# Kernel optimization log

Measured on AMD Instinct MI355X. Metric: run time of the kernel, lower is better.

The kernel has to match this reference:

```python
import jax, jax.numpy as jnp
import numpy as np

N_NODES, D = 10000, 128
N_EDGES = 640000
BN_EPS = 1e-3  # keras BatchNormalization default


def _bn(x, gamma, beta, mean, var):
    return (x - mean) * jax.lax.rsqrt(var + BN_EPS) * gamma + beta


def _ffn_block(x, gamma, beta, mean, var, W, b):
    # BatchNorm (inference) -> Dropout (identity at inference) -> Dense + gelu (exact, keras default)
    return jax.nn.gelu(_bn(x, gamma, beta, mean, var) @ W + b, approximate=False)


def setup_inputs() -> dict:
    key = jax.random.key(0)
    ks = jax.random.split(key, 32)
    inp = {
        "node_features": jax.random.normal(ks[0], (N_NODES, D), jnp.float32),
        "edges": jax.random.randint(ks[1], (2, N_EDGES), 0, N_NODES, jnp.int64),
        "edge_weights": jax.random.uniform(ks[2], (N_EDGES,), jnp.float32),
    }
    def bn_params(i, dim, prefix):
        return {
            prefix + "_g": jnp.ones((dim,), jnp.float32) + 0.1 * jax.random.normal(ks[i], (dim,)),
            prefix + "_b": 0.1 * jax.random.normal(ks[i + 1], (dim,)),
            prefix + "_m": 0.1 * jax.random.normal(ks[i + 2], (dim,)),
            prefix + "_v": jax.random.uniform(ks[i + 3], (dim,), minval=0.5, maxval=1.5),
        }
    def dense_params(i, din, dout, prefix):
        s = (2.0 / (din + dout)) ** 0.5
        return {
            prefix + "_W": s * jax.random.normal(ks[i], (din, dout), jnp.float32),
            prefix + "_bias": jnp.zeros((dout,), jnp.float32),
        }
    # prepare FFN: BN(D)->Dense(D->128), BN(128)->Dense(128->128)
    inp.update(bn_params(3, D, "p1")); inp.update(dense_params(7, D, 128, "p1"))
    inp.update(bn_params(8, 128, "p2")); inp.update(dense_params(12, 128, 128, "p2"))
    # update FFN (concat -> 2*D input): BN(2D)->Dense(2D->128), BN(128)->Dense(128->128)
    inp.update(bn_params(13, 2 * D, "u1")); inp.update(dense_params(17, 2 * D, 128, "u1"))
    inp.update(bn_params(18, 128, "u2")); inp.update(dense_params(22, 128, 128, "u2"))
    return inp


def reference(node_features, edges, edge_weights,
              p1_g, p1_b, p1_m, p1_v, p1_W, p1_bias,
              p2_g, p2_b, p2_m, p2_v, p2_W, p2_bias,
              u1_g, u1_b, u1_m, u1_v, u1_W, u1_bias,
              u2_g, u2_b, u2_m, u2_v, u2_W, u2_bias):
    num_nodes = node_features.shape[0]
    node_idx, nbr_idx = edges[0], edges[1]
    # gather neighbor representations [E, D]
    neigh = node_features[nbr_idx]
    # prepare: ffn on neighbors, then scale by edge weights
    msg = _ffn_block(neigh, p1_g, p1_b, p1_m, p1_v, p1_W, p1_bias)
    msg = _ffn_block(msg, p2_g, p2_b, p2_m, p2_v, p2_W, p2_bias)
    msg = msg * edge_weights[:, None]
    # aggregate: unsorted_segment_mean
    agg = jax.ops.segment_sum(msg, node_idx, num_segments=num_nodes)
    cnt = jax.ops.segment_sum(jnp.ones_like(edge_weights), node_idx, num_segments=num_nodes)
    agg = agg / jnp.maximum(cnt, 1.0)[:, None]
    # update: concat + ffn
    h = jnp.concatenate([node_features, agg], axis=1)
    h = _ffn_block(h, u1_g, u1_b, u1_m, u1_v, u1_W, u1_bias)
    h = _ffn_block(h, u2_g, u2_b, u2_m, u2_v, u2_W, u2_bias)
    return h
```

## Files before the change

kernel.cpp:

```cpp
#include <hip/hip_runtime.h>
#include <hip/hip_bf16.h>
#include <hip/hip_fp16.h>
#include <math.h>

#define N_NODES 10000
#define DIM 128
#define N_EDGES 640000
#define BN_EPS 1e-3f

#define QUARTER 2500
#define PART_BLOCKS 250
#define EDGES_PER_PART 2560
#define HIST_GRID 1000
#define MSG64_BLOCKS 157
#define SU_BLOCKS 1250
#define HIST_PAD 10240

typedef _Float16 half8 __attribute__((ext_vector_type(8)));
typedef float f32x4 __attribute__((ext_vector_type(4)));

__device__ __forceinline__ float gelu_exact(float x) {
  return 0.5f * x * (1.0f + erff(x * 0.70710678f));
}

__device__ __forceinline__ int lds_swz(int row, int colbyte) {
  return ((row * 256 + colbyte) ^ ((row & 7) << 4));
}

struct FoldAll {
  const float* g[4];
  const float* bb[4];
  const float* m[4];
  const float* v[4];
  const float* W[4];
  const float* bias[4];
  _Float16* pk[4];
  float* bf[4];
  int din[4];
  int S[4];
};

__global__ __launch_bounds__(256) void fold_hist_kernel(FoldAll fa,
                                                        const int* __restrict__ node_idx,
                                                        unsigned char* __restrict__ part) {
  __shared__ int lh[QUARTER];
  __shared__ float t_sh[256];
  __shared__ float bpart[128];
  int b = blockIdx.x, t = threadIdx.x;
  if (b >= 44) {
    int pb = b - 44;
    int eb = pb >> 2;
    int q = pb & 3;
    int qbase = q * QUARTER;
    for (int i = t; i < QUARTER; i += 256) lh[i] = 0;
    __syncthreads();
    int base0 = eb * EDGES_PER_PART;
#pragma unroll
    for (int s = 0; s < 3; ++s) {
      int off = s * 1024 + t * 4;
      if (off < EDGES_PER_PART) {
        int4 vv = *reinterpret_cast<const int4*>(&node_idx[base0 + off]);
        unsigned d0 = (unsigned)(vv.x - qbase);
        unsigned d1 = (unsigned)(vv.y - qbase);
        unsigned d2 = (unsigned)(vv.z - qbase);
        unsigned d3 = (unsigned)(vv.w - qbase);
        if (d0 < QUARTER) atomicAdd(&lh[d0], 1);
        if (d1 < QUARTER) atomicAdd(&lh[d1], 1);
        if (d2 < QUARTER) atomicAdd(&lh[d2], 1);
        if (d3 < QUARTER) atomicAdd(&lh[d3], 1);
      }
    }
    __syncthreads();
    unsigned char* prow = part + (size_t)(q * PART_BLOCKS + eb) * QUARTER;
    for (int i = t; i < QUARTER; i += 256) prow[i] = (unsigned char)lh[i];
    return;
  }
  if (b >= 40) {
    int p = b - 40;
    int din = fa.din[p];
    const float* W = fa.W[p];
    for (int k = t; k < din; k += 256) {
      float sc = fa.g[p][k] * rsqrtf(fa.v[p][k] + BN_EPS);
      t_sh[k] = fa.bb[p][k] - fa.m[p][k] * sc;
    }
    __syncthreads();
    int j = t & 127, kh = t >> 7;
    int half = din >> 1;
    float acc = 0.f;
    for (int k = kh * half; k < (kh + 1) * half; ++k)
      acc = fmaf(t_sh[k], W[k * 128 + j], acc);
    if (kh == 1) bpart[j] = acc;
    __syncthreads();
    if (kh == 0) fa.bf[p][j] = acc + bpart[j] + fa.bias[p][j];
    return;
  }
  int p, lf;
  if (b < 8)       { p = 0; lf = b * 256 + t; }
  else if (b < 16) { p = 1; lf = (b - 8) * 256 + t; }
  else if (b < 32) { p = 2; lf = (b - 16) * 256 + t; }
  else             { p = 3; lf = (b - 32) * 256 + t; }
  int S = fa.S[p];
  int l = lf & 63;
  int fs = lf >> 6;
  int f = fs & 7, s = fs >> 3;
  if (s >= S) return;
  const float* W = fa.W[p];
  const float* g = fa.g[p];
  const float* v = fa.v[p];
  int k0 = s * 32 + (l >> 4) * 8;
  int col = f * 16 + (l & 15);
  half8 h;
#pragma unroll
  for (int i = 0; i < 8; ++i) {
    int k = k0 + i;
    float sc = g[k] * rsqrtf(v[k] + BN_EPS);
    h[i] = (_Float16)(sc * W[k * 128 + col]);
  }
  *reinterpret_cast<half8*>(fa.pk[p] + (size_t)lf * 8) = h;
}

__global__ __launch_bounds__(256) void merge_msg_kernel(
    unsigned char* __restrict__ part, int* __restrict__ hist,
    const float* __restrict__ x,
    const _Float16* __restrict__ W1pk, const float* __restrict__ b1f,
    const _Float16* __restrict__ W2pk, const float* __restrict__ b2f,
    _Float16* __restrict__ M) {
  __shared__ char lds_raw[4 * 4096];
  int b = blockIdx.x, t = threadIdx.x;
  if (b < 40) {
    int bin = b * 256 + t;
    if (bin < N_NODES) {
      int q = bin / QUARTER;
      int bp = bin - q * QUARTER;
      unsigned char* col = part + (size_t)q * PART_BLOCKS * QUARTER + bp;
      int sum = 0;
#pragma unroll
      for (int c = 0; c < PART_BLOCKS; c += 25) {
        int vals[25];
#pragma unroll
        for (int i = 0; i < 25; ++i) vals[i] = col[(size_t)(c + i) * QUARTER];
#pragma unroll
        for (int i = 0; i < 25; ++i) {
          col[(size_t)(c + i) * QUARTER] = (unsigned char)sum;
          sum += vals[i];
        }
      }
      hist[bin] = sum;
    } else if (bin < HIST_PAD) {
      hist[bin] = 0;
    }
    return;
  }
  int wid = t >> 6, lane = t & 63;
  int r = lane & 15, g = lane >> 4;
  int row0 = (b - 40) * 64 + wid * 16;
  char* lbase = lds_raw + wid * 4096;

  int arow = row0 + r;
  if (arow > N_NODES - 1) arow = N_NODES - 1;
  const float* xp = x + (size_t)arow * DIM;

  half8 a[4];
#pragma unroll
  for (int s = 0; s < 4; ++s) {
    float4 lo = *reinterpret_cast<const float4*>(xp + s * 32 + g * 8);
    float4 hi = *reinterpret_cast<const float4*>(xp + s * 32 + g * 8 + 4);
    half8 h;
    h[0] = (_Float16)lo.x; h[1] = (_Float16)lo.y; h[2] = (_Float16)lo.z; h[3] = (_Float16)lo.w;
    h[4] = (_Float16)hi.x; h[5] = (_Float16)hi.y; h[6] = (_Float16)hi.z; h[7] = (_Float16)hi.w;
    a[s] = h;
  }

  f32x4 zero = {0.f, 0.f, 0.f, 0.f};
  f32x4 acc[8];
#pragma unroll
  for (int f = 0; f < 8; ++f) acc[f] = zero;
#pragma unroll
  for (int f = 0; f < 8; ++f)
#pragma unroll
    for (int s = 0; s < 4; ++s) {
      half8 bfrag = *reinterpret_cast<const half8*>(W1pk + (size_t)((s * 8 + f) * 64 + lane) * 8);
      acc[f] = __builtin_amdgcn_mfma_f32_16x16x32_f16(a[s], bfrag, acc[f], 0, 0, 0);
    }

#pragma unroll
  for (int f = 0; f < 8; ++f) {
    int col = f * 16 + r;
    float bv = b1f[col];
#pragma unroll
    for (int j = 0; j < 4; ++j) {
      int rl = g * 4 + j;
      float gv = gelu_exact(acc[f][j] + bv);
      *reinterpret_cast<_Float16*>(lbase + lds_swz(rl, col * 2)) = (_Float16)gv;
    }
  }

  half8 a2[4];
#pragma unroll
  for (int s = 0; s < 4; ++s)
    a2[s] = *reinterpret_cast<const half8*>(lbase + lds_swz(r, (s * 32 + g * 8) * 2));

  f32x4 acc2[8];
#pragma unroll
  for (int f = 0; f < 8; ++f) acc2[f] = zero;
#pragma unroll
  for (int f = 0; f < 8; ++f)
#pragma unroll
    for (int s = 0; s < 4; ++s) {
      half8 bfrag = *reinterpret_cast<const half8*>(W2pk + (size_t)((s * 8 + f) * 64 + lane) * 8);
      acc2[f] = __builtin_amdgcn_mfma_f32_16x16x32_f16(a2[s], bfrag, acc2[f], 0, 0, 0);
    }

#pragma unroll
  for (int f = 0; f < 8; ++f) {
    int col = f * 16 + r;
    float bv = b2f[col];
#pragma unroll
    for (int j = 0; j < 4; ++j) {
      int grow = row0 + g * 4 + j;
      if (grow < N_NODES)
        M[(size_t)grow * DIM + col] = (_Float16)gelu_exact(acc2[f][j] + bv);
    }
  }
}

__global__ __launch_bounds__(256) void scatter_kernel(
    const int* __restrict__ node_idx, const int* __restrict__ nbr_idx,
    const float* __restrict__ ew, const int* __restrict__ hist,
    const unsigned char* __restrict__ part, uint2* __restrict__ edge_s,
    int* __restrict__ row_start) {
  __shared__ int cur[QUARTER];
  __shared__ int sums[256];
  int bk = blockIdx.x, t = threadIdx.x;
  int eb = bk >> 2;
  int q = bk & 3;
  int qbase = q * QUARTER;
  const int PER = 40;
  int i0 = t * PER;
  int lh[PER];
  int total = 0;
#pragma unroll
  for (int i = 0; i < PER; i += 4) {
    int4 h4 = *reinterpret_cast<const int4*>(&hist[i0 + i]);
    lh[i] = h4.x; lh[i + 1] = h4.y; lh[i + 2] = h4.z; lh[i + 3] = h4.w;
    total += h4.x + h4.y + h4.z + h4.w;
  }
  sums[t] = total;
  __syncthreads();
  for (int off = 1; off < 256; off <<= 1) {
    int v = (t >= off) ? sums[t - off] : 0;
    __syncthreads();
    sums[t] += v;
    __syncthreads();
  }
  int running = sums[t] - total;
  const unsigned char* prow = part + (size_t)(q * PART_BLOCKS + eb) * QUARTER;
  bool wrs = (bk == 0);
#pragma unroll
  for (int i = 0; i < PER; ++i) {
    int idx = i0 + i;
    if (idx < N_NODES) {
      unsigned d = (unsigned)(idx - qbase);
      if (d < QUARTER) cur[d] = running + (int)prow[d];
      if (wrs) row_start[idx] = running;
      running += lh[i];
    }
  }
  if (wrs && t == 255) row_start[N_NODES] = running;
  __syncthreads();

  int base0 = eb * EDGES_PER_PART;
#pragma unroll
  for (int s = 0; s < 3; ++s) {
    int off = s * 1024 + t * 4;
    if (off >= EDGES_PER_PART) break;
    int base = base0 + off;
    int4 ni = *reinterpret_cast<const int4*>(&node_idx[base]);
    int4 nb = *reinterpret_cast<const int4*>(&nbr_idx[base]);
    float4 wv = *reinterpret_cast<const float4*>(&ew[base]);
    unsigned d0 = (unsigned)(ni.x - qbase);
    unsigned d1 = (unsigned)(ni.y - qbase);
    unsigned d2 = (unsigned)(ni.z - qbase);
    unsigned d3 = (unsigned)(ni.w - qbase);
    if (d0 < QUARTER) {
      int p0 = atomicAdd(&cur[d0], 1);
      edge_s[p0] = make_uint2((unsigned)nb.x, __float_as_uint(wv.x));
    }
    if (d1 < QUARTER) {
      int p1 = atomicAdd(&cur[d1], 1);
      edge_s[p1] = make_uint2((unsigned)nb.y, __float_as_uint(wv.y));
    }
    if (d2 < QUARTER) {
      int p2 = atomicAdd(&cur[d2], 1);
      edge_s[p2] = make_uint2((unsigned)nb.z, __float_as_uint(wv.z));
    }
    if (d3 < QUARTER) {
      int p3 = atomicAdd(&cur[d3], 1);
      edge_s[p3] = make_uint2((unsigned)nb.w, __float_as_uint(wv.w));
    }
  }
}

__global__ __launch_bounds__(512) void spmm_update_kernel(
    const int* __restrict__ row_start, const uint2* __restrict__ edge_s,
    const __half* __restrict__ M, const float* __restrict__ x,
    const _Float16* __restrict__ U1pk, const float* __restrict__ bu1,
    const _Float16* __restrict__ U2pk, const float* __restrict__ bu2,
    float* __restrict__ out) {
  __shared__ float scratch[3][8][128];
  __shared__ char tile[4096];
  int t = threadIdx.x;
  int row0 = blockIdx.x * 8;

  {
    int r = t >> 6;
    int q = t & 63;
    int slice = q >> 4;
    int sub = q & 15;
    int row = row0 + r;
    int s = row_start[row];
    int e_end = row_start[row + 1];
    float acc[8];
#pragma unroll
    for (int c = 0; c < 8; ++c) acc[c] = 0.f;
    const __half* Mb = M + sub * 8;
    for (int base = s + slice * 8; base < e_end; base += 32) {
      uint2 pk[8];
#pragma unroll
      for (int k = 0; k < 8; ++k) {
        int e = base + k;
        pk[k] = edge_s[(e < e_end) ? e : s];
        if (e >= e_end) pk[k].y = 0u;
      }
      uint4 raw[8];
#pragma unroll
      for (int k = 0; k < 8; ++k)
        raw[k] = *reinterpret_cast<const uint4*>(Mb + (size_t)pk[k].x * DIM);
#pragma unroll
      for (int k = 0; k < 8; ++k) {
        float w = __uint_as_float(pk[k].y);
        const __half2* h2 = reinterpret_cast<const __half2*>(&raw[k]);
#pragma unroll
        for (int qq = 0; qq < 4; ++qq) {
          float2 f = __half22float2(h2[qq]);
          acc[2 * qq] = fmaf(w, f.x, acc[2 * qq]);
          acc[2 * qq + 1] = fmaf(w, f.y, acc[2 * qq + 1]);
        }
      }
    }
    if (slice >= 1) {
      *reinterpret_cast<float4*>(&scratch[slice - 1][r][sub * 8]) =
          make_float4(acc[0], acc[1], acc[2], acc[3]);
      *reinterpret_cast<float4*>(&scratch[slice - 1][r][sub * 8 + 4]) =
          make_float4(acc[4], acc[5], acc[6], acc[7]);
    }
    __syncthreads();
    if (slice == 0) {
#pragma unroll
      for (int sl = 0; sl < 3; ++sl) {
        float4 o0 = *reinterpret_cast<const float4*>(&scratch[sl][r][sub * 8]);
        float4 o1 = *reinterpret_cast<const float4*>(&scratch[sl][r][sub * 8 + 4]);
        acc[0] += o0.x; acc[1] += o0.y; acc[2] += o0.z; acc[3] += o0.w;
        acc[4] += o1.x; acc[5] += o1.y; acc[6] += o1.z; acc[7] += o1.w;
      }
      int cnt = e_end - s;
      float inv = 1.f / (float)(cnt > 0 ? cnt : 1);
      half8 h;
#pragma unroll
      for (int c = 0; c < 8; ++c) h[c] = (_Float16)(acc[c] * inv);
      *reinterpret_cast<half8*>(tile + lds_swz(r, sub * 16)) = h;
    }
  }
  __syncthreads();

  int wid = t >> 6, lane = t & 63;
  bool act = wid < 4;
  int r = lane & 15, g = lane >> 4;
  half8 hzero;
#pragma unroll
  for (int i = 0; i < 8; ++i) hzero[i] = (_Float16)0.f;

  half8 a[8];
#pragma unroll
  for (int s = 0; s < 8; ++s) a[s] = hzero;
  if (act && r < 8) {
    const float* xp = x + (size_t)(row0 + r) * DIM;
#pragma unroll
    for (int s = 0; s < 4; ++s) {
      float4 lo = *reinterpret_cast<const float4*>(xp + s * 32 + g * 8);
      float4 hi = *reinterpret_cast<const float4*>(xp + s * 32 + g * 8 + 4);
      half8 h;
      h[0] = (_Float16)lo.x; h[1] = (_Float16)lo.y; h[2] = (_Float16)lo.z; h[3] = (_Float16)lo.w;
      h[4] = (_Float16)hi.x; h[5] = (_Float16)hi.y; h[6] = (_Float16)hi.z; h[7] = (_Float16)hi.w;
      a[s] = h;
    }
#pragma unroll
    for (int s = 0; s < 4; ++s)
      a[4 + s] = *reinterpret_cast<const half8*>(tile + lds_swz(r, (s * 32 + g * 8) * 2));
  }
  __syncthreads();

  f32x4 zero = {0.f, 0.f, 0.f, 0.f};
  if (act) {
    f32x4 acc1[2];
    acc1[0] = zero; acc1[1] = zero;
#pragma unroll
    for (int fi = 0; fi < 2; ++fi) {
      int f = wid * 2 + fi;
#pragma unroll
      for (int s = 0; s < 8; ++s) {
        half8 bfrag = *reinterpret_cast<const half8*>(U1pk + (size_t)((s * 8 + f) * 64 + lane) * 8);
        acc1[fi] = __builtin_amdgcn_mfma_f32_16x16x32_f16(a[s], bfrag, acc1[fi], 0, 0, 0);
      }
    }
#pragma unroll
    for (int fi = 0; fi < 2; ++fi) {
      int f = wid * 2 + fi;
      int col = f * 16 + r;
      float bv = bu1[col];
#pragma unroll
      for (int j = 0; j < 4; ++j) {
        int rl = g * 4 + j;
        float gv = gelu_exact(acc1[fi][j] + bv);
        *reinterpret_cast<_Float16*>(tile + lds_swz(rl, col * 2)) = (_Float16)gv;
      }
    }
  }
  __syncthreads();

  if (act) {
    half8 a2[4];
#pragma unroll
    for (int s = 0; s < 4; ++s) a2[s] = hzero;
    if (r < 8) {
#pragma unroll
      for (int s = 0; s < 4; ++s)
        a2[s] = *reinterpret_cast<const half8*>(tile + lds_swz(r, (s * 32 + g * 8) * 2));
    }
    f32x4 acc2[2];
    acc2[0] = zero; acc2[1] = zero;
#pragma unroll
    for (int fi = 0; fi < 2; ++fi) {
      int f = wid * 2 + fi;
#pragma unroll
      for (int s = 0; s < 4; ++s) {
        half8 bfrag = *reinterpret_cast<const half8*>(U2pk + (size_t)((s * 8 + f) * 64 + lane) * 8);
        acc2[fi] = __builtin_amdgcn_mfma_f32_16x16x32_f16(a2[s], bfrag, acc2[fi], 0, 0, 0);
      }
    }
#pragma unroll
    for (int fi = 0; fi < 2; ++fi) {
      int f = wid * 2 + fi;
      int col = f * 16 + r;
      float bv = bu2[col];
#pragma unroll
      for (int j = 0; j < 4; ++j) {
        int rloc = g * 4 + j;
        if (rloc < 8)
          out[(size_t)(row0 + rloc) * DIM + col] = gelu_exact(acc2[fi][j] + bv);
      }
    }
  }
}

extern "C" void kernel_launch(void* const* d_in, const int* in_sizes, int n_in,
                              void* d_out, int out_size, void* d_ws, size_t ws_size,
                              hipStream_t stream) {
  const float* x = (const float*)d_in[0];
  const int* edges = (const int*)d_in[1];
  const float* ew = (const float*)d_in[2];

  const int* node_idx = edges;
  const int* nbr_idx = edges + N_EDGES;

  char* wsp = (char*)d_ws;
  auto alloc = [&](size_t bytes) {
    char* p = wsp;
    wsp += (bytes + 255) & ~(size_t)255;
    return p;
  };
  _Float16* M = (_Float16*)alloc((size_t)N_NODES * DIM * 2);
  _Float16* W1pk = (_Float16*)alloc(128 * 128 * 2);
  _Float16* W2pk = (_Float16*)alloc(128 * 128 * 2);
  _Float16* U1pk = (_Float16*)alloc(256 * 128 * 2);
  _Float16* U2pk = (_Float16*)alloc(128 * 128 * 2);
  float* b1f = (float*)alloc(128 * 4);
  float* b2f = (float*)alloc(128 * 4);
  float* bu1 = (float*)alloc(128 * 4);
  float* bu2 = (float*)alloc(128 * 4);
  int* hist = (int*)alloc(HIST_PAD * 4);
  int* row_start = (int*)alloc((N_NODES + 1) * 4);
  unsigned char* part = (unsigned char*)alloc((size_t)PART_BLOCKS * N_NODES);
  uint2* edge_s = (uint2*)alloc((size_t)N_EDGES * 8);

  FoldAll fa;
  fa.g[0] = (const float*)d_in[3];  fa.bb[0] = (const float*)d_in[4];
  fa.m[0] = (const float*)d_in[5];  fa.v[0] = (const float*)d_in[6];
  fa.W[0] = (const float*)d_in[7];  fa.bias[0] = (const float*)d_in[8];
  fa.g[1] = (const float*)d_in[9];  fa.bb[1] = (const float*)d_in[10];
  fa.m[1] = (const float*)d_in[11]; fa.v[1] = (const float*)d_in[12];
  fa.W[1] = (const float*)d_in[13]; fa.bias[1] = (const float*)d_in[14];
  fa.g[2] = (const float*)d_in[15]; fa.bb[2] = (const float*)d_in[16];
  fa.m[2] = (const float*)d_in[17]; fa.v[2] = (const float*)d_in[18];
  fa.W[2] = (const float*)d_in[19]; fa.bias[2] = (const float*)d_in[20];
  fa.g[3] = (const float*)d_in[21]; fa.bb[3] = (const float*)d_in[22];
  fa.m[3] = (const float*)d_in[23]; fa.v[3] = (const float*)d_in[24];
  fa.W[3] = (const float*)d_in[25]; fa.bias[3] = (const float*)d_in[26];
  fa.pk[0] = W1pk; fa.pk[1] = W2pk; fa.pk[2] = U1pk; fa.pk[3] = U2pk;
  fa.bf[0] = b1f; fa.bf[1] = b2f; fa.bf[2] = bu1; fa.bf[3] = bu2;
  fa.din[0] = 128; fa.din[1] = 128; fa.din[2] = 256; fa.din[3] = 128;
  fa.S[0] = 4; fa.S[1] = 4; fa.S[2] = 8; fa.S[3] = 4;

  fold_hist_kernel<<<44 + HIST_GRID, 256, 0, stream>>>(fa, node_idx, part);
  merge_msg_kernel<<<40 + MSG64_BLOCKS, 256, 0, stream>>>(
      part, hist, x, W1pk, b1f, W2pk, b2f, M);
  scatter_kernel<<<HIST_GRID, 256, 0, stream>>>(
      node_idx, nbr_idx, ew, hist, part, edge_s, row_start);
  spmm_update_kernel<<<SU_BLOCKS, 512, 0, stream>>>(
      row_start, edge_s, (const __half*)M, x, U1pk, bu1, U2pk, bu2, (float*)d_out);
}
```

Before: 114.6 us.

## Use full-range LDS histogram blocks and shrink spmm-update blocks to 256 threads

The histogram stage now has each block count all 10000 destination nodes in a 40KB LDS array, rather than splitting them into four quarter-range blocks, which cuts the block count by four and removes the redundant re-reads of node_idx. The spmm/update kernel drops from 512 to 256 threads per block. Each thread now gathers 16 halves (two 16-byte loads) per edge and covers 4 edges per slice, and the four waves that used to sit idle during the MFMA stage are removed. The larger LDS use may lower histogram occupancy, and having fewer threads per row in the gather reduces memory-level parallelism.

```diff
diff --git a/kernel.cpp b/kernel.cpp
--- a/kernel.cpp
+++ b/kernel.cpp
@@ -11,7 +11,7 @@
 #define QUARTER 2500
 #define PART_BLOCKS 250
 #define EDGES_PER_PART 2560
-#define HIST_GRID 1000
+#define SCAT_GRID 1000
 #define MSG64_BLOCKS 157
 #define SU_BLOCKS 1250
 #define HIST_PAD 10240
@@ -43,16 +43,13 @@
 __global__ __launch_bounds__(256) void fold_hist_kernel(FoldAll fa,
                                                         const int* __restrict__ node_idx,
                                                         unsigned char* __restrict__ part) {
-  __shared__ int lh[QUARTER];
+  __shared__ int lh[N_NODES];
   __shared__ float t_sh[256];
   __shared__ float bpart[128];
   int b = blockIdx.x, t = threadIdx.x;
   if (b >= 44) {
-    int pb = b - 44;
-    int eb = pb >> 2;
-    int q = pb & 3;
-    int qbase = q * QUARTER;
-    for (int i = t; i < QUARTER; i += 256) lh[i] = 0;
+    int eb = b - 44;
+    for (int i = t; i < N_NODES; i += 256) lh[i] = 0;
     __syncthreads();
     int base0 = eb * EDGES_PER_PART;
 #pragma unroll
@@ -60,19 +57,18 @@
       int off = s * 1024 + t * 4;
       if (off < EDGES_PER_PART) {
         int4 vv = *reinterpret_cast<const int4*>(&node_idx[base0 + off]);
-        unsigned d0 = (unsigned)(vv.x - qbase);
-        unsigned d1 = (unsigned)(vv.y - qbase);
-        unsigned d2 = (unsigned)(vv.z - qbase);
-        unsigned d3 = (unsigned)(vv.w - qbase);
-        if (d0 < QUARTER) atomicAdd(&lh[d0], 1);
-        if (d1 < QUARTER) atomicAdd(&lh[d1], 1);
-        if (d2 < QUARTER) atomicAdd(&lh[d2], 1);
-        if (d3 < QUARTER) atomicAdd(&lh[d3], 1);
-      }
-    }
-    __syncthreads();
-    unsigned char* prow = part + (size_t)(q * PART_BLOCKS + eb) * QUARTER;
-    for (int i = t; i < QUARTER; i += 256) prow[i] = (unsigned char)lh[i];
+        atomicAdd(&lh[vv.x], 1);
+        atomicAdd(&lh[vv.y], 1);
+        atomicAdd(&lh[vv.z], 1);
+        atomicAdd(&lh[vv.w], 1);
+      }
+    }
+    __syncthreads();
+    for (int i = t; i < N_NODES; i += 256) {
+      int q = i / QUARTER;
+      int bp = i - q * QUARTER;
+      part[(size_t)(q * PART_BLOCKS + eb) * QUARTER + bp] = (unsigned char)lh[i];
+    }
     return;
   }
   if (b >= 40) {
@@ -301,7 +297,7 @@
   }
 }
 
-__global__ __launch_bounds__(512) void spmm_update_kernel(
+__global__ __launch_bounds__(256) void spmm_update_kernel(
     const int* __restrict__ row_start, const uint2* __restrict__ edge_s,
     const __half* __restrict__ M, const float* __restrict__ x,
     const _Float16* __restrict__ U1pk, const float* __restrict__ bu1,
@@ -313,35 +309,38 @@
   int row0 = blockIdx.x * 8;
 
   {
-    int r = t >> 6;
-    int q = t & 63;
-    int slice = q >> 4;
-    int sub = q & 15;
+    int r = t >> 5;
+    int q = t & 31;
+    int slice = q >> 3;
+    int sub = q & 7;
     int row = row0 + r;
     int s = row_start[row];
     int e_end = row_start[row + 1];
-    float acc[8];
-#pragma unroll
-    for (int c = 0; c < 8; ++c) acc[c] = 0.f;
-    const __half* Mb = M + sub * 8;
-    for (int base = s + slice * 8; base < e_end; base += 32) {
-      uint2 pk[8];
-#pragma unroll
-      for (int k = 0; k < 8; ++k) {
+    float acc[16];
+#pragma unroll
+    for (int c = 0; c < 16; ++c) acc[c] = 0.f;
+    const __half* Mb = M + sub * 16;
+    for (int base = s + slice * 4; base < e_end; base += 16) {
+      uint2 pk[4];
+#pragma unroll
+      for (int k = 0; k < 4; ++k) {
         int e = base + k;
         pk[k] = edge_s[(e < e_end) ? e : s];
         if (e >= e_end) pk[k].y = 0u;
       }
       uint4 raw[8];
 #pragma unroll
-      for (int k = 0; k < 8; ++k)
-        raw[k] = *reinterpret_cast<const uint4*>(Mb + (size_t)pk[k].x * DIM);
-#pragma unroll
-      for (int k = 0; k < 8; ++k) {
+      for (int k = 0; k < 4; ++k) {
+        const uint4* mp = reinterpret_cast<const uint4*>(Mb + (size_t)pk[k].x * DIM);
+        raw[2 * k] = mp[0];
+        raw[2 * k + 1] = mp[1];
+      }
+#pragma unroll
+      for (int k = 0; k < 4; ++k) {
         float w = __uint_as_float(pk[k].y);
-        const __half2* h2 = reinterpret_cast<const __half2*>(&raw[k]);
-#pragma unroll
-        for (int qq = 0; qq < 4; ++qq) {
+        const __half2* h2 = reinterpret_cast<const __half2*>(&raw[2 * k]);
+#pragma unroll
+        for (int qq = 0; qq < 8; ++qq) {
           float2 f = __half22float2(h2[qq]);
           acc[2 * qq] = fmaf(w, f.x, acc[2 * qq]);
           acc[2 * qq + 1] = fmaf(w, f.y, acc[2 * qq + 1]);
@@ -349,32 +348,37 @@
       }
     }
     if (slice >= 1) {
-      *reinterpret_cast<float4*>(&scratch[slice - 1][r][sub * 8]) =
-          make_float4(acc[0], acc[1], acc[2], acc[3]);
-      *reinterpret_cast<float4*>(&scratch[slice - 1][r][sub * 8 + 4]) =
-          make_float4(acc[4], acc[5], acc[6], acc[7]);
+      float* dst = &scratch[slice - 1][r][sub * 16];
+      *reinterpret_cast<float4*>(dst) = make_float4(acc[0], acc[1], acc[2], acc[3]);
+      *reinterpret_cast<float4*>(dst + 4) = make_float4(acc[4], acc[5], acc[6], acc[7]);
+      *reinterpret_cast<float4*>(dst + 8) = make_float4(acc[8], acc[9], acc[10], acc[11]);
+      *reinterpret_cast<float4*>(dst + 12) = make_float4(acc[12], acc[13], acc[14], acc[15]);
     }
     __syncthreads();
     if (slice == 0) {
 #pragma unroll
       for (int sl = 0; sl < 3; ++sl) {
-        float4 o0 = *reinterpret_cast<const float4*>(&scratch[sl][r][sub * 8]);
-        float4 o1 = *reinterpret_cast<const float4*>(&scratch[sl][r][sub * 8 + 4]);
-        acc[0] += o0.x; acc[1] += o0.y; acc[2] += o0.z; acc[3] += o0.w;
-        acc[4] += o1.x; acc[5] += o1.y; acc[6] += o1.z; acc[7] += o1.w;
+        const float* src = &scratch[sl][r][sub * 16];
+#pragma unroll
+        for (int c = 0; c < 16; c += 4) {
+          float4 o = *reinterpret_cast<const float4*>(src + c);
+          acc[c] += o.x; acc[c + 1] += o.y; acc[c + 2] += o.z; acc[c + 3] += o.w;
+        }
       }
       int cnt = e_end - s;
       float inv = 1.f / (float)(cnt > 0 ? cnt : 1);
-      half8 h;
-#pragma unroll
-      for (int c = 0; c < 8; ++c) h[c] = (_Float16)(acc[c] * inv);
-      *reinterpret_cast<half8*>(tile + lds_swz(r, sub * 16)) = h;
+      half8 hlo, hhi;
+#pragma unroll
+      for (int c = 0; c < 8; ++c) hlo[c] = (_Float16)(acc[c] * inv);
+#pragma unroll
+      for (int c = 0; c < 8; ++c) hhi[c] = (_Float16)(acc[8 + c] * inv);
+      *reinterpret_cast<half8*>(tile + lds_swz(r, sub * 32)) = hlo;
+      *reinterpret_cast<half8*>(tile + lds_swz(r, sub * 32 + 16)) = hhi;
     }
   }
   __syncthreads();
 
   int wid = t >> 6, lane = t & 63;
-  bool act = wid < 4;
   int r = lane & 15, g = lane >> 4;
   half8 hzero;
 #pragma unroll
@@ -383,7 +387,7 @@
   half8 a[8];
 #pragma unroll
   for (int s = 0; s < 8; ++s) a[s] = hzero;
-  if (act && r < 8) {
+  if (r < 8) {
     const float* xp = x + (size_t)(row0 + r) * DIM;
 #pragma unroll
     for (int s = 0; s < 4; ++s) {
@@ -401,7 +405,7 @@
   __syncthreads();
 
   f32x4 zero = {0.f, 0.f, 0.f, 0.f};
-  if (act) {
+  {
     f32x4 acc1[2];
     acc1[0] = zero; acc1[1] = zero;
 #pragma unroll
@@ -428,7 +432,7 @@
   }
   __syncthreads();
 
-  if (act) {
+  {
     half8 a2[4];
 #pragma unroll
     for (int s = 0; s < 4; ++s) a2[s] = hzero;
@@ -511,11 +515,11 @@
   fa.din[0] = 128; fa.din[1] = 128; fa.din[2] = 256; fa.din[3] = 128;
   fa.S[0] = 4; fa.S[1] = 4; fa.S[2] = 8; fa.S[3] = 4;
 
-  fold_hist_kernel<<<44 + HIST_GRID, 256, 0, stream>>>(fa, node_idx, part);
+  fold_hist_kernel<<<44 + PART_BLOCKS, 256, 0, stream>>>(fa, node_idx, part);
   merge_msg_kernel<<<40 + MSG64_BLOCKS, 256, 0, stream>>>(
       part, hist, x, W1pk, b1f, W2pk, b2f, M);
-  scatter_kernel<<<HIST_GRID, 256, 0, stream>>>(
+  scatter_kernel<<<SCAT_GRID, 256, 0, stream>>>(
       node_idx, nbr_idx, ew, hist, part, edge_s, row_start);
-  spmm_update_kernel<<<SU_BLOCKS, 512, 0, stream>>>(
+  spmm_update_kernel<<<SU_BLOCKS, 256, 0, stream>>>(
       row_start, edge_s, (const __half*)M, x, U1pk, bu1, U2pk, bu2, (float*)d_out);
 }
```

After: 108.1 us. 1.06x faster.
